# Performance work log

Hardware: AMD Instinct MI355X
Metric: run time of the kernel (lower is better)

The kernel has to match this reference:

```python
import jax, jax.numpy as jnp
import numpy as np

HEAD_DIM = 128
NUM_QUERY_GROUPS = 4
BLOCK_SIZE = 64
NUM_SELECTED = 16


def setup_inputs() -> dict:
    key = jax.random.key(0)
    k1, k2, k3, k4 = jax.random.split(key, 4)
    query = jax.random.normal(k1, (4, 32, 1, 128), jnp.float32)
    compressed_keys = jax.random.normal(k2, (4, 32, 128, 128), jnp.float32)
    keys = jax.random.normal(k3, (4, 4, 8192, 128), jnp.float32)
    values = jax.random.normal(k4, (4, 4, 8192, 128), jnp.float32)
    return {"query": query, "compressed_keys": compressed_keys, "keys": keys, "values": values}


def reference(query, compressed_keys, keys, values):
    # --- compressed attention importance scores ---
    q = query[:, :, -1, :]                                     # [B, H, D] (last query position)
    scale = 1.0 / (HEAD_DIM ** 0.5)
    scores = jnp.einsum('bhd,bhnd->bhn', q, compressed_keys) * scale  # [B, H, N]
    probs = jax.nn.softmax(scores, axis=-1)
    # --- GQA pooling: mean over heads within each query group ---
    B, H, N = probs.shape
    probs = probs.reshape(B, NUM_QUERY_GROUPS, H // NUM_QUERY_GROUPS, N).mean(axis=2)  # [B, G, N]
    # --- top-k block selection ---
    _, idx = jax.lax.top_k(probs, NUM_SELECTED)                # [B, G, n]
    block_starts = idx * BLOCK_SIZE                            # [B, G, n]
    offsets = jnp.arange(BLOCK_SIZE, dtype=block_starts.dtype)
    gather_idx = (block_starts[..., None] + offsets).reshape(B, NUM_QUERY_GROUPS, NUM_SELECTED * BLOCK_SIZE)  # [B, G, n*bs]
    # --- gather whole K/V blocks ---
    selected_keys = jnp.take_along_axis(keys, gather_idx[..., None], axis=2)    # [B, G, n*bs, D]
    selected_values = jnp.take_along_axis(values, gather_idx[..., None], axis=2)
    return selected_keys, selected_values
```

## Files before the change

kernel.cpp:

```cpp
#include <hip/hip_runtime.h>
#include <math.h>

#define BB   4
#define HH   32
#define GG   4
#define HPG  8
#define DD   128
#define NCK  128
#define SEQ  8192
#define NSEL 16
#define BLK  64

__global__ __launch_bounds__(512, 1) void gemv_kernel(const float* __restrict__ query,
                                                      const float* __restrict__ ck,
                                                      float* __restrict__ scores_out) {
    const int blk  = blockIdx.x;
    const int bh   = blk >> 1;
    const int half = blk & 1;
    const int t    = threadIdx.x;
    const int r    = (t >> 3) + half * 64;
    const int sub  = t & 7;

    __shared__ float q_sh[DD];
    if (t < DD) q_sh[t] = query[(size_t)bh * DD + t];
    __syncthreads();

    const float4* c4 = (const float4*)(ck + ((size_t)bh * NCK + r) * DD) + sub;
    const float4* q4 = ((const float4*)q_sh) + sub;
    float s = 0.0f;
    #pragma unroll
    for (int i = 0; i < 4; ++i) {
        float4 a = q4[i * 8];
        float4 c = c4[i * 8];
        s += a.x * c.x + a.y * c.y + a.z * c.z + a.w * c.w;
    }
    s += __shfl_xor(s, 1);
    s += __shfl_xor(s, 2);
    s += __shfl_xor(s, 4);

    if (sub == 0) scores_out[(size_t)bh * NCK + r] = s * 0.08838834764831845f;
}

__global__ __launch_bounds__(512, 1) void select_gather_kernel(const float* __restrict__ scores,
                                                               const float* __restrict__ keys,
                                                               const float* __restrict__ values,
                                                               float* __restrict__ out) {
    const int bid  = blockIdx.x;
    const int bg   = bid >> 4;
    const int sown = bid & 15;
    const int b    = bg >> 2;
    const int g    = bg & 3;
    const int t    = threadIdx.x;
    const int w    = t >> 6;

    __shared__ float redm[2][HPG];
    __shared__ float reds[2][HPG];
    __shared__ float pm[NCK];
    __shared__ int   sel_sh;

    float sc[HPG];
    float e[HPG];

    if (t < NCK) {
        #pragma unroll
        for (int j = 0; j < HPG; ++j)
            sc[j] = scores[(size_t)(b * HH + g * HPG + j) * NCK + t];
        #pragma unroll
        for (int j = 0; j < HPG; ++j) {
            float m = sc[j];
            #pragma unroll
            for (int off = 1; off < 64; off <<= 1) m = fmaxf(m, __shfl_xor(m, off));
            if ((t & 63) == 0) redm[w][j] = m;
        }
    }
    __syncthreads();

    if (t < NCK) {
        #pragma unroll
        for (int j = 0; j < HPG; ++j) {
            const float m = fmaxf(redm[0][j], redm[1][j]);
            e[j] = expf(sc[j] - m);
            float ssum = e[j];
            #pragma unroll
            for (int off = 1; off < 64; off <<= 1) ssum += __shfl_xor(ssum, off);
            if ((t & 63) == 0) reds[w][j] = ssum;
        }
    }
    __syncthreads();

    if (t < NCK) {
        float p = 0.0f;
        #pragma unroll
        for (int j = 0; j < HPG; ++j) p += e[j] / (reds[0][j] + reds[1][j]);
        pm[t] = p * 0.125f;
    }
    __syncthreads();

    if (t < NCK) {
        const float mv = pm[t];
        int rank = 0;
        for (int i = 0; i < NCK; ++i) {
            const float vi = pm[i];
            if (vi > mv || (vi == mv && i < t)) ++rank;
        }
        if (rank == sown) sel_sh = t;
    }
    __syncthreads();
    const int sel = sel_sh;

    const size_t src  = ((size_t)bg * SEQ + (size_t)sel * BLK) * DD;
    const size_t dst  = ((size_t)bg * (NSEL * BLK) + (size_t)sown * BLK) * DD;
    const size_t VOFF = (size_t)BB * GG * NSEL * BLK * DD;

    const float4* ks = (const float4*)(keys + src);
    const float4* vs = (const float4*)(values + src);
    float4* kd = (float4*)(out + dst);
    float4* vd = (float4*)(out + VOFF + dst);

    #pragma unroll
    for (int i = 0; i < 4; ++i) kd[i * 512 + t] = ks[i * 512 + t];
    #pragma unroll
    for (int i = 0; i < 4; ++i) vd[i * 512 + t] = vs[i * 512 + t];
}

extern "C" void kernel_launch(void* const* d_in, const int* in_sizes, int n_in,
                              void* d_out, int out_size, void* d_ws, size_t ws_size,
                              hipStream_t stream) {
    const float* query  = (const float*)d_in[0];
    const float* ck     = (const float*)d_in[1];
    const float* keys   = (const float*)d_in[2];
    const float* values = (const float*)d_in[3];
    float* out = (float*)d_out;

    float* scores = (float*)d_ws;

    gemv_kernel<<<BB * HH * 2, 512, 0, stream>>>(query, ck, scores);
    select_gather_kernel<<<BB * GG * NSEL, 512, 0, stream>>>(scores, keys, values, out);
}
```

Measured before the change: 22.15 us.

## Compute top-k selection once per group and split K/V gather into separate blocks

Moves the score GEMV, softmax, head pooling and ranking into one selector kernel per (batch, group) that writes block indices. The 16 blocks that each recomputed the selection no longer do so. A separate gather kernel copies either K or V per block, doubling the copy parallelism. The trade-off is that the compressed-key GEMV now runs on only 16 blocks, which may limit the bandwidth available for that stage.

```diff
diff --git a/kernel.cpp b/kernel.cpp
--- a/kernel.cpp
+++ b/kernel.cpp
@@ -11,89 +11,80 @@
 #define NSEL 16
 #define BLK  64
 
-__global__ __launch_bounds__(512, 1) void gemv_kernel(const float* __restrict__ query,
-                                                      const float* __restrict__ ck,
-                                                      float* __restrict__ scores_out) {
-    const int blk  = blockIdx.x;
-    const int bh   = blk >> 1;
-    const int half = blk & 1;
-    const int t    = threadIdx.x;
-    const int r    = (t >> 3) + half * 64;
-    const int sub  = t & 7;
+__global__ __launch_bounds__(1024, 1) void selector_kernel(const float* __restrict__ query,
+                                                           const float* __restrict__ ck,
+                                                           int* __restrict__ idx_out) {
+    const int bg = blockIdx.x;
+    const int b  = bg >> 2;
+    const int g  = bg & 3;
+    const int t  = threadIdx.x;
+    const int r  = t >> 3;
+    const int sub = t & 7;
+    const int w  = t >> 6;
 
-    __shared__ float q_sh[DD];
-    if (t < DD) q_sh[t] = query[(size_t)bh * DD + t];
-    __syncthreads();
+    __shared__ float q_sh[HPG][DD];
+    __shared__ float redm[16][HPG];
+    __shared__ float reds[16][HPG];
+    __shared__ float pm[NCK];
 
-    const float4* c4 = (const float4*)(ck + ((size_t)bh * NCK + r) * DD) + sub;
-    const float4* q4 = ((const float4*)q_sh) + sub;
-    float s = 0.0f;
-    #pragma unroll
-    for (int i = 0; i < 4; ++i) {
-        float4 a = q4[i * 8];
-        float4 c = c4[i * 8];
-        s += a.x * c.x + a.y * c.y + a.z * c.z + a.w * c.w;
-    }
-    s += __shfl_xor(s, 1);
-    s += __shfl_xor(s, 2);
-    s += __shfl_xor(s, 4);
-
-    if (sub == 0) scores_out[(size_t)bh * NCK + r] = s * 0.08838834764831845f;
-}
-
-__global__ __launch_bounds__(512, 1) void select_gather_kernel(const float* __restrict__ scores,
-                                                               const float* __restrict__ keys,
-                                                               const float* __restrict__ values,
-                                                               float* __restrict__ out) {
-    const int bid  = blockIdx.x;
-    const int bg   = bid >> 4;
-    const int sown = bid & 15;
-    const int b    = bg >> 2;
-    const int g    = bg & 3;
-    const int t    = threadIdx.x;
-    const int w    = t >> 6;
-
-    __shared__ float redm[2][HPG];
-    __shared__ float reds[2][HPG];
-    __shared__ float pm[NCK];
-    __shared__ int   sel_sh;
-
-    float sc[HPG];
-    float e[HPG];
-
-    if (t < NCK) {
-        #pragma unroll
-        for (int j = 0; j < HPG; ++j)
-            sc[j] = scores[(size_t)(b * HH + g * HPG + j) * NCK + t];
-        #pragma unroll
-        for (int j = 0; j < HPG; ++j) {
-            float m = sc[j];
-            #pragma unroll
-            for (int off = 1; off < 64; off <<= 1) m = fmaxf(m, __shfl_xor(m, off));
-            if ((t & 63) == 0) redm[w][j] = m;
-        }
+    {
+        const int j = t >> 7, d = t & 127;
+        q_sh[j][d] = query[(size_t)(b * HH + g * HPG + j) * DD + d];
     }
     __syncthreads();
 
-    if (t < NCK) {
+    float sc[HPG];
+    const size_t base = ((size_t)(b * HH + g * HPG) * NCK + r) * DD;
+    #pragma unroll
+    for (int j = 0; j < HPG; ++j) {
+        const float4* c4 = (const float4*)(ck + base + (size_t)j * NCK * DD) + sub;
+        const float4* q4 = ((const float4*)&q_sh[j][0]) + sub;
+        float s = 0.0f;
         #pragma unroll
-        for (int j = 0; j < HPG; ++j) {
-            const float m = fmaxf(redm[0][j], redm[1][j]);
-            e[j] = expf(sc[j] - m);
-            float ssum = e[j];
-            #pragma unroll
-            for (int off = 1; off < 64; off <<= 1) ssum += __shfl_xor(ssum, off);
-            if ((t & 63) == 0) reds[w][j] = ssum;
+        for (int i = 0; i < 4; ++i) {
+            float4 a = q4[i * 8];
+            float4 c = c4[i * 8];
+            s += a.x * c.x + a.y * c.y + a.z * c.z + a.w * c.w;
         }
+        s += __shfl_xor(s, 1);
+        s += __shfl_xor(s, 2);
+        s += __shfl_xor(s, 4);
+        sc[j] = s * 0.08838834764831845f;
+    }
+
+    #pragma unroll
+    for (int j = 0; j < HPG; ++j) {
+        float m = sc[j];
+        #pragma unroll
+        for (int off = 1; off < 64; off <<= 1) m = fmaxf(m, __shfl_xor(m, off));
+        if ((t & 63) == 0) redm[w][j] = m;
     }
     __syncthreads();
 
-    if (t < NCK) {
-        float p = 0.0f;
+    float e[HPG];
+    #pragma unroll
+    for (int j = 0; j < HPG; ++j) {
+        float m = redm[0][j];
         #pragma unroll
-        for (int j = 0; j < HPG; ++j) p += e[j] / (reds[0][j] + reds[1][j]);
-        pm[t] = p * 0.125f;
+        for (int ww = 1; ww < 16; ++ww) m = fmaxf(m, redm[ww][j]);
+        e[j] = expf(sc[j] - m);
+        float ssum = e[j];
+        #pragma unroll
+        for (int off = 1; off < 64; off <<= 1) ssum += __shfl_xor(ssum, off);
+        if ((t & 63) == 0) reds[w][j] = ssum;
     }
+    __syncthreads();
+
+    float p = 0.0f;
+    #pragma unroll
+    for (int j = 0; j < HPG; ++j) {
+        float S8 = reds[0][j];
+        #pragma unroll
+        for (int ww = 1; ww < 16; ++ww) S8 += reds[ww][j];
+        p += 8.0f * e[j] / S8;
+    }
+    p *= 0.125f;
+    if (sub == 0) pm[r] = p;
     __syncthreads();
 
     if (t < NCK) {
@@ -103,24 +94,32 @@
             const float vi = pm[i];
             if (vi > mv || (vi == mv && i < t)) ++rank;
         }
-        if (rank == sown) sel_sh = t;
+        if (rank < NSEL) idx_out[bg * NSEL + rank] = t;
     }
-    __syncthreads();
-    const int sel = sel_sh;
+}
+
+__global__ __launch_bounds__(512, 1) void gather_kernel(const float* __restrict__ keys,
+                                                        const float* __restrict__ values,
+                                                        const int* __restrict__ idx,
+                                                        float* __restrict__ out) {
+    const int bid = blockIdx.x;
+    const int isV = bid & 1;
+    const int bs  = bid >> 1;
+    const int bg  = bs >> 4;
+    const int s   = bs & 15;
+    const int t   = threadIdx.x;
+
+    const int sel = idx[bs];
 
     const size_t src  = ((size_t)bg * SEQ + (size_t)sel * BLK) * DD;
-    const size_t dst  = ((size_t)bg * (NSEL * BLK) + (size_t)sown * BLK) * DD;
+    const size_t dst  = ((size_t)bg * (NSEL * BLK) + (size_t)s * BLK) * DD;
     const size_t VOFF = (size_t)BB * GG * NSEL * BLK * DD;
 
-    const float4* ks = (const float4*)(keys + src);
-    const float4* vs = (const float4*)(values + src);
-    float4* kd = (float4*)(out + dst);
-    float4* vd = (float4*)(out + VOFF + dst);
+    const float4* sp = (const float4*)((isV ? values : keys) + src);
+    float4*       dp = (float4*)(out + (isV ? VOFF : 0) + dst);
 
     #pragma unroll
-    for (int i = 0; i < 4; ++i) kd[i * 512 + t] = ks[i * 512 + t];
-    #pragma unroll
-    for (int i = 0; i < 4; ++i) vd[i * 512 + t] = vs[i * 512 + t];
+    for (int i = 0; i < 4; ++i) dp[i * 512 + t] = sp[i * 512 + t];
 }
 
 extern "C" void kernel_launch(void* const* d_in, const int* in_sizes, int n_in,
@@ -132,8 +131,8 @@
     const float* values = (const float*)d_in[3];
     float* out = (float*)d_out;
 
-    float* scores = (float*)d_ws;
+    int* idx = (int*)d_ws;
 
-    gemv_kernel<<<BB * HH * 2, 512, 0, stream>>>(query, ck, scores);
-    select_gather_kernel<<<BB * GG * NSEL, 512, 0, stream>>>(scores, keys, values, out);
+    selector_kernel<<<BB * GG, 1024, 0, stream>>>(query, ck, idx);
+    gather_kernel<<<BB * GG * NSEL * 2, 512, 0, stream>>>(keys, values, idx, out);
 }
```

Measured after the change: 30.64 us. +38.3%, slower.

## Split fused select-gather into separate top-k and wide gather kernels

Applied to the files above, without the earlier changes.

The previous fused kernel recomputed the softmax, GQA pooling and rank-based top-k in every one of its 256 blocks before copying one K/V block. This change computes the top-k indices once per (batch, group) in a small kernel that writes them to workspace. A separate gather kernel then uses four times as many smaller blocks, each copying half a block of either keys or values. This removes redundant per-block selection work and the latency it added before the copy, and it increases memory-level parallelism. The cost is an extra kernel launch and a dependency through global memory.

```diff
diff --git a/kernel.cpp b/kernel.cpp
--- a/kernel.cpp
+++ b/kernel.cpp
@@ -41,86 +41,82 @@
     if (sub == 0) scores_out[(size_t)bh * NCK + r] = s * 0.08838834764831845f;
 }
 
-__global__ __launch_bounds__(512, 1) void select_gather_kernel(const float* __restrict__ scores,
-                                                               const float* __restrict__ keys,
-                                                               const float* __restrict__ values,
-                                                               float* __restrict__ out) {
-    const int bid  = blockIdx.x;
-    const int bg   = bid >> 4;
-    const int sown = bid & 15;
-    const int b    = bg >> 2;
-    const int g    = bg & 3;
-    const int t    = threadIdx.x;
-    const int w    = t >> 6;
+__global__ __launch_bounds__(128, 1) void topk_kernel(const float* __restrict__ scores,
+                                                      int* __restrict__ idx_out) {
+    const int bg = blockIdx.x;
+    const int b  = bg >> 2;
+    const int g  = bg & 3;
+    const int t  = threadIdx.x;
+    const int w  = t >> 6;
 
     __shared__ float redm[2][HPG];
     __shared__ float reds[2][HPG];
     __shared__ float pm[NCK];
-    __shared__ int   sel_sh;
 
     float sc[HPG];
     float e[HPG];
 
-    if (t < NCK) {
+    #pragma unroll
+    for (int j = 0; j < HPG; ++j)
+        sc[j] = scores[(size_t)(b * HH + g * HPG + j) * NCK + t];
+
+    #pragma unroll
+    for (int j = 0; j < HPG; ++j) {
+        float m = sc[j];
         #pragma unroll
-        for (int j = 0; j < HPG; ++j)
-            sc[j] = scores[(size_t)(b * HH + g * HPG + j) * NCK + t];
-        #pragma unroll
-        for (int j = 0; j < HPG; ++j) {
-            float m = sc[j];
-            #pragma unroll
-            for (int off = 1; off < 64; off <<= 1) m = fmaxf(m, __shfl_xor(m, off));
-            if ((t & 63) == 0) redm[w][j] = m;
-        }
+        for (int off = 1; off < 64; off <<= 1) m = fmaxf(m, __shfl_xor(m, off));
+        if ((t & 63) == 0) redm[w][j] = m;
     }
     __syncthreads();
 
-    if (t < NCK) {
+    #pragma unroll
+    for (int j = 0; j < HPG; ++j) {
+        const float m = fmaxf(redm[0][j], redm[1][j]);
+        e[j] = expf(sc[j] - m);
+        float ssum = e[j];
         #pragma unroll
-        for (int j = 0; j < HPG; ++j) {
-            const float m = fmaxf(redm[0][j], redm[1][j]);
-            e[j] = expf(sc[j] - m);
-            float ssum = e[j];
-            #pragma unroll
-            for (int off = 1; off < 64; off <<= 1) ssum += __shfl_xor(ssum, off);
-            if ((t & 63) == 0) reds[w][j] = ssum;
-        }
+        for (int off = 1; off < 64; off <<= 1) ssum += __shfl_xor(ssum, off);
+        if ((t & 63) == 0) reds[w][j] = ssum;
     }
     __syncthreads();
 
-    if (t < NCK) {
-        float p = 0.0f;
-        #pragma unroll
-        for (int j = 0; j < HPG; ++j) p += e[j] / (reds[0][j] + reds[1][j]);
-        pm[t] = p * 0.125f;
-    }
+    float p = 0.0f;
+    #pragma unroll
+    for (int j = 0; j < HPG; ++j) p += e[j] / (reds[0][j] + reds[1][j]);
+    pm[t] = p * 0.125f;
     __syncthreads();
 
-    if (t < NCK) {
-        const float mv = pm[t];
-        int rank = 0;
-        for (int i = 0; i < NCK; ++i) {
-            const float vi = pm[i];
-            if (vi > mv || (vi == mv && i < t)) ++rank;
-        }
-        if (rank == sown) sel_sh = t;
+    const float mv = pm[t];
+    int rank = 0;
+    for (int i = 0; i < NCK; ++i) {
+        const float vi = pm[i];
+        if (vi > mv || (vi == mv && i < t)) ++rank;
     }
-    __syncthreads();
-    const int sel = sel_sh;
+    if (rank < NSEL) idx_out[bg * NSEL + rank] = t;
+}
 
-    const size_t src  = ((size_t)bg * SEQ + (size_t)sel * BLK) * DD;
-    const size_t dst  = ((size_t)bg * (NSEL * BLK) + (size_t)sown * BLK) * DD;
+__global__ __launch_bounds__(256, 1) void gather_kernel(const float* __restrict__ keys,
+                                                        const float* __restrict__ values,
+                                                        const int* __restrict__ idx,
+                                                        float* __restrict__ out) {
+    const int bid  = blockIdx.x;
+    const int isV  = bid & 1;
+    const int half = (bid >> 1) & 1;
+    const int s    = (bid >> 2) & 15;
+    const int bg   = bid >> 6;
+    const int t    = threadIdx.x;
+
+    const int sel = idx[bg * NSEL + s];
+
+    const size_t src  = ((size_t)bg * SEQ + (size_t)sel * BLK + half * 32) * DD;
+    const size_t dst  = ((size_t)bg * (NSEL * BLK) + (size_t)s * BLK + half * 32) * DD;
     const size_t VOFF = (size_t)BB * GG * NSEL * BLK * DD;
 
-    const float4* ks = (const float4*)(keys + src);
-    const float4* vs = (const float4*)(values + src);
-    float4* kd = (float4*)(out + dst);
-    float4* vd = (float4*)(out + VOFF + dst);
+    const float4* sp = (const float4*)((isV ? values : keys) + src);
+    float4*       dp = (float4*)(out + (isV ? VOFF : 0) + dst);
 
     #pragma unroll
-    for (int i = 0; i < 4; ++i) kd[i * 512 + t] = ks[i * 512 + t];
-    #pragma unroll
-    for (int i = 0; i < 4; ++i) vd[i * 512 + t] = vs[i * 512 + t];
+    for (int i = 0; i < 4; ++i) dp[i * 256 + t] = sp[i * 256 + t];
 }
 
 extern "C" void kernel_launch(void* const* d_in, const int* in_sizes, int n_in,
@@ -133,7 +129,9 @@
     float* out = (float*)d_out;
 
     float* scores = (float*)d_ws;
+    int*   idx    = (int*)((char*)d_ws + (size_t)BB * HH * NCK * sizeof(float));
 
     gemv_kernel<<<BB * HH * 2, 512, 0, stream>>>(query, ck, scores);
-    select_gather_kernel<<<BB * GG * NSEL, 512, 0, stream>>>(scores, keys, values, out);
+    topk_kernel<<<BB * GG, 128, 0, stream>>>(scores, idx);
+    gather_kernel<<<BB * GG * NSEL * 4, 256, 0, stream>>>(keys, values, idx, out);
 }
```

After: 23.63 us. 1.07x slower.

## Split gather across K/V and half-blocks; drop softmax max subtraction

Applied to the files above, without the earlier changes.

The gather grid is split four ways: each block now copies either keys or values for half of one selected block, with 256 threads per block instead of 512. This raises parallelism across CUs for the memory copy. The softmax also drops the max-subtraction pass and its barrier, and removes the constant mean scale, which does not affect the ranking. In exchange, every block redundantly recomputes the top-k selection, and expf may overflow for large scores.

```diff
diff --git a/kernel.cpp b/kernel.cpp
--- a/kernel.cpp
+++ b/kernel.cpp
@@ -41,45 +41,33 @@
     if (sub == 0) scores_out[(size_t)bh * NCK + r] = s * 0.08838834764831845f;
 }
 
-__global__ __launch_bounds__(512, 1) void select_gather_kernel(const float* __restrict__ scores,
+__global__ __launch_bounds__(256, 1) void select_gather_kernel(const float* __restrict__ scores,
                                                                const float* __restrict__ keys,
                                                                const float* __restrict__ values,
                                                                float* __restrict__ out) {
     const int bid  = blockIdx.x;
-    const int bg   = bid >> 4;
-    const int sown = bid & 15;
+    const int q2   = bid & 3;
+    const int isV  = q2 >> 1;
+    const int half = q2 & 1;
+    const int s    = (bid >> 2) & 15;
+    const int bg   = bid >> 6;
     const int b    = bg >> 2;
     const int g    = bg & 3;
     const int t    = threadIdx.x;
     const int w    = t >> 6;
 
-    __shared__ float redm[2][HPG];
     __shared__ float reds[2][HPG];
     __shared__ float pm[NCK];
     __shared__ int   sel_sh;
 
-    float sc[HPG];
     float e[HPG];
 
     if (t < NCK) {
         #pragma unroll
         for (int j = 0; j < HPG; ++j)
-            sc[j] = scores[(size_t)(b * HH + g * HPG + j) * NCK + t];
+            e[j] = expf(scores[(size_t)(b * HH + g * HPG + j) * NCK + t]);
         #pragma unroll
         for (int j = 0; j < HPG; ++j) {
-            float m = sc[j];
-            #pragma unroll
-            for (int off = 1; off < 64; off <<= 1) m = fmaxf(m, __shfl_xor(m, off));
-            if ((t & 63) == 0) redm[w][j] = m;
-        }
-    }
-    __syncthreads();
-
-    if (t < NCK) {
-        #pragma unroll
-        for (int j = 0; j < HPG; ++j) {
-            const float m = fmaxf(redm[0][j], redm[1][j]);
-            e[j] = expf(sc[j] - m);
             float ssum = e[j];
             #pragma unroll
             for (int off = 1; off < 64; off <<= 1) ssum += __shfl_xor(ssum, off);
@@ -92,7 +80,7 @@
         float p = 0.0f;
         #pragma unroll
         for (int j = 0; j < HPG; ++j) p += e[j] / (reds[0][j] + reds[1][j]);
-        pm[t] = p * 0.125f;
+        pm[t] = p;
     }
     __syncthreads();
 
@@ -103,24 +91,20 @@
             const float vi = pm[i];
             if (vi > mv || (vi == mv && i < t)) ++rank;
         }
-        if (rank == sown) sel_sh = t;
+        if (rank == s) sel_sh = t;
     }
     __syncthreads();
     const int sel = sel_sh;
 
-    const size_t src  = ((size_t)bg * SEQ + (size_t)sel * BLK) * DD;
-    const size_t dst  = ((size_t)bg * (NSEL * BLK) + (size_t)sown * BLK) * DD;
+    const size_t src  = ((size_t)bg * SEQ + (size_t)sel * BLK + half * 32) * DD;
+    const size_t dst  = ((size_t)bg * (NSEL * BLK) + (size_t)s * BLK + half * 32) * DD;
     const size_t VOFF = (size_t)BB * GG * NSEL * BLK * DD;
 
-    const float4* ks = (const float4*)(keys + src);
-    const float4* vs = (const float4*)(values + src);
-    float4* kd = (float4*)(out + dst);
-    float4* vd = (float4*)(out + VOFF + dst);
+    const float4* sp = (const float4*)((isV ? values : keys) + src);
+    float4*       dp = (float4*)(out + (isV ? VOFF : 0) + dst);
 
     #pragma unroll
-    for (int i = 0; i < 4; ++i) kd[i * 512 + t] = ks[i * 512 + t];
-    #pragma unroll
-    for (int i = 0; i < 4; ++i) vd[i * 512 + t] = vs[i * 512 + t];
+    for (int i = 0; i < 4; ++i) dp[i * 256 + t] = sp[i * 256 + t];
 }
 
 extern "C" void kernel_launch(void* const* d_in, const int* in_sizes, int n_in,
@@ -135,5 +119,5 @@
     float* scores = (float*)d_ws;
 
     gemv_kernel<<<BB * HH * 2, 512, 0, stream>>>(query, ck, scores);
-    select_gather_kernel<<<BB * GG * NSEL, 512, 0, stream>>>(scores, keys, values, out);
+    select_gather_kernel<<<BB * GG * NSEL * 4, 256, 0, stream>>>(scores, keys, values, out);
 }
```

Measured after the change: 20.13 us. -9.1%, faster.
